# Kernel optimization log

Measured on AMD Instinct MI355X. Metric: run time of the kernel, lower is better.

## Reference

```python
import jax, jax.numpy as jnp
import numpy as np

B = 8192          # batch size
D = 1024          # embedding dim
N_CLASSES = 7     # 7 emotion labels


def setup_inputs() -> dict:
    key = jax.random.key(0)
    k1, k2, k3, k4 = jax.random.split(key, 4)
    return {
        "label": jax.random.randint(k1, (B,), 0, N_CLASSES),
        "s_t": jax.random.normal(k2, (B, D), dtype=jnp.float32),
        "s_v": jax.random.normal(k3, (B, D), dtype=jnp.float32),
        "s_a": jax.random.normal(k4, (B, D), dtype=jnp.float32),
    }


def _single_modal_loss(label, anchor, a_cls, a_m, m_1, m_2):
    # anchor embedding and its norm
    anc = a_m[anchor]                                  # [D]
    anc_norm = jnp.linalg.norm(anc)
    # batched cosine similarity of anchor vs every row of m_1 and m_2
    def cos(m):
        return (m @ anc) / (jnp.linalg.norm(m, axis=1) * anc_norm)  # [B]
    c = cos(m_1) + cos(m_2)                            # [B]
    not_anchor = jnp.arange(label.shape[0]) != anchor
    same = label == label[anchor]
    pos_mask = not_anchor & same
    neg_mask = not_anchor & ~same
    # original code normalizes by full class count (anchor included)
    pos_num = jnp.sum(label == a_cls).astype(c.dtype)
    neg_num = label.shape[0] - pos_num
    pos_score = jnp.sum(jnp.where(pos_mask, c, 0.0)) / pos_num
    neg_score = jnp.sum(jnp.where(neg_mask, c, 0.0)) / neg_num
    return 2.0 - pos_score + neg_score


def reference(label, s_t, s_v, s_a):
    # first class (starting from 0) with more than one sample, like the while loop
    counts = jax.ops.segment_sum(jnp.ones_like(label), label, num_segments=N_CLASSES)
    a_cls = jnp.argmax(counts > 1)
    # deterministic anchor: first index of that class
    anchor = jnp.argmax(label == a_cls)
    t1 = _single_modal_loss(label, anchor, a_cls, s_t, s_v, s_a)
    t2 = _single_modal_loss(label, anchor, a_cls, s_a, s_t, s_v)
    t3 = _single_modal_loss(label, anchor, a_cls, s_v, s_a, s_t)
    return (t1 + t2 + t3) / 3.0
```

## Files before the change

kernel.cpp:

```cpp
#include <hip/hip_runtime.h>

#define NCLS 7

struct Hdr {
    int   anchor;
    int   a_cls;
    float pos_num;
    float neg_num;
    float inv_at;
    float inv_av;
    float inv_aa;
    int   pad;
};

__device__ __forceinline__ float dot4(float4 a, float4 b) {
    return a.x * b.x + a.y * b.y + a.z * b.z + a.w * b.w;
}

__device__ __forceinline__ float wave_fsum_dpp(float x) {
    float t;
    t = __int_as_float(__builtin_amdgcn_update_dpp(0, __float_as_int(x), 0x111, 0xf, 0xf, true));  x += t;
    t = __int_as_float(__builtin_amdgcn_update_dpp(0, __float_as_int(x), 0x112, 0xf, 0xf, true));  x += t;
    t = __int_as_float(__builtin_amdgcn_update_dpp(0, __float_as_int(x), 0x114, 0xf, 0xf, true));  x += t;
    t = __int_as_float(__builtin_amdgcn_update_dpp(0, __float_as_int(x), 0x118, 0xf, 0xf, true));  x += t;
    t = __int_as_float(__builtin_amdgcn_update_dpp(0, __float_as_int(x), 0x142, 0xa, 0xf, false)); x += t;
    t = __int_as_float(__builtin_amdgcn_update_dpp(0, __float_as_int(x), 0x143, 0xc, 0xf, false)); x += t;
    return __int_as_float(__builtin_amdgcn_readlane(__float_as_int(x), 63));
}

__device__ __forceinline__ int wave_isum_dpp(int x) {
    int t;
    t = __builtin_amdgcn_update_dpp(0, x, 0x111, 0xf, 0xf, true);  x += t;
    t = __builtin_amdgcn_update_dpp(0, x, 0x112, 0xf, 0xf, true);  x += t;
    t = __builtin_amdgcn_update_dpp(0, x, 0x114, 0xf, 0xf, true);  x += t;
    t = __builtin_amdgcn_update_dpp(0, x, 0x118, 0xf, 0xf, true);  x += t;
    t = __builtin_amdgcn_update_dpp(0, x, 0x142, 0xa, 0xf, false); x += t;
    t = __builtin_amdgcn_update_dpp(0, x, 0x143, 0xc, 0xf, false); x += t;
    return __builtin_amdgcn_readlane(x, 63);
}

__device__ __forceinline__ int wave_imin_dpp(int x) {
    const int I = 0x7fffffff;
    int t;
    t = __builtin_amdgcn_update_dpp(I, x, 0x111, 0xf, 0xf, false); x = min(x, t);
    t = __builtin_amdgcn_update_dpp(I, x, 0x112, 0xf, 0xf, false); x = min(x, t);
    t = __builtin_amdgcn_update_dpp(I, x, 0x114, 0xf, 0xf, false); x = min(x, t);
    t = __builtin_amdgcn_update_dpp(I, x, 0x118, 0xf, 0xf, false); x = min(x, t);
    t = __builtin_amdgcn_update_dpp(I, x, 0x142, 0xa, 0xf, false); x = min(x, t);
    t = __builtin_amdgcn_update_dpp(I, x, 0x143, 0xc, 0xf, false); x = min(x, t);
    return __builtin_amdgcn_readlane(x, 63);
}

__global__ __launch_bounds__(1024) void prep_kernel(
    const int* __restrict__ label,
    const float* __restrict__ s_t,
    const float* __restrict__ s_v,
    const float* __restrict__ s_a,
    int B, int D, float* __restrict__ ws)
{
    const int tid  = threadIdx.x;
    const int w    = tid >> 6;
    const int lane = tid & 63;

    int cnt[NCLS];
    int mn[NCLS];
#pragma unroll
    for (int k = 0; k < NCLS; ++k) { cnt[k] = 0; mn[k] = 0x7fffffff; }

    const int4* lab4 = (const int4*)label;
    const int n4 = B >> 2;
    for (int j = tid; j < n4; j += 1024) {
        int4 L = lab4[j];
        const int base = j << 2;
        int ls[4] = { L.x, L.y, L.z, L.w };
#pragma unroll
        for (int e = 0; e < 4; ++e) {
#pragma unroll
            for (int k = 0; k < NCLS; ++k) {
                if (ls[e] == k) { cnt[k]++; mn[k] = min(mn[k], base + e); }
            }
        }
    }
    for (int i = (n4 << 2) + tid; i < B; i += 1024) {
        int l = label[i];
#pragma unroll
        for (int k = 0; k < NCLS; ++k)
            if (l == k) { cnt[k]++; mn[k] = min(mn[k], i); }
    }

#pragma unroll
    for (int k = 0; k < NCLS; ++k) {
        cnt[k] = wave_isum_dpp(cnt[k]);
        mn[k]  = wave_imin_dpp(mn[k]);
    }

    __shared__ int   s_cnt[16][NCLS], s_mn[16][NCLS];
    __shared__ int   s_anchor;
    __shared__ float s_norm[12];
    if (lane == 0) {
#pragma unroll
        for (int k = 0; k < NCLS; ++k) { s_cnt[w][k] = cnt[k]; s_mn[w][k] = mn[k]; }
    }
    __syncthreads();

    if (tid == 0) {
        int hist[NCLS], mini[NCLS];
#pragma unroll
        for (int k = 0; k < NCLS; ++k) {
            int hc = 0, mc = 0x7fffffff;
            for (int q = 0; q < 16; ++q) { hc += s_cnt[q][k]; mc = min(mc, s_mn[q][k]); }
            hist[k] = hc; mini[k] = mc;
        }
        int c = 0;
#pragma unroll
        for (int k = NCLS - 1; k >= 0; --k) if (hist[k] > 1) c = k;
        s_anchor = mini[c];

        Hdr* h = (Hdr*)ws;
        h->anchor  = mini[c];
        h->a_cls   = c;
        float pn   = (float)hist[c];
        h->pos_num = pn;
        h->neg_num = (float)B - pn;
    }
    __syncthreads();

    const int anchor = s_anchor;
    if (w < 12) {
        const int rw = w >> 2, qw = w & 3;
        const float* src = (rw == 0) ? s_t : (rw == 1) ? s_v : s_a;
        const float4* row = (const float4*)(src + (size_t)anchor * D);
        const int nvec = D >> 2;
        float s = 0.f;
        for (int j = qw * 64 + lane; j < nvec; j += 256) {
            float4 x = row[j];
            s += dot4(x, x);
        }
        s = wave_fsum_dpp(s);
        if (lane == 0) s_norm[w] = s;
    }
    __syncthreads();
    if (tid < 3)
        ((float*)ws)[4 + tid] = rsqrtf(s_norm[4 * tid] + s_norm[4 * tid + 1] +
                                       s_norm[4 * tid + 2] + s_norm[4 * tid + 3]);
}

__global__ __launch_bounds__(256, 8) void main_kernel(
    const int* __restrict__ label,
    const float* __restrict__ s_t,
    const float* __restrict__ s_v,
    const float* __restrict__ s_a,
    int B, int D, float* __restrict__ ws)
{
    const Hdr* h = (const Hdr*)ws;
    float2* partials = (float2*)(ws + 16);

    const int lane = threadIdx.x & 63;
    const int r    = blockIdx.x * 4 + (threadIdx.x >> 6);
    if (r >= B) return;

    const int anchor = h->anchor;
    const int lab    = label[r];

    const float4* rt = (const float4*)(s_t + (size_t)r * D);
    const float4* rv = (const float4*)(s_v + (size_t)r * D);
    const float4* ra = (const float4*)(s_a + (size_t)r * D);
    const float4* at = (const float4*)(s_t + (size_t)anchor * D);
    const float4* av = (const float4*)(s_v + (size_t)anchor * D);
    const float4* aa = (const float4*)(s_a + (size_t)anchor * D);

    float dt_a = 0.f, dt_v = 0.f, sq_t = 0.f;
    float dv_t = 0.f, dv_a = 0.f, sq_v = 0.f;
    float da_t = 0.f, da_v = 0.f, sq_a = 0.f;

    const int nvec = D >> 2;
#pragma unroll 1
    for (int j = lane; j < nvec; j += 64) {
        float4 t  = rt[j], v  = rv[j], a  = ra[j];
        float4 bt = at[j], bv = av[j], ba = aa[j];
        dt_a += dot4(t, ba);  dt_v += dot4(t, bv);  sq_t += dot4(t, t);
        dv_t += dot4(v, bt);  dv_a += dot4(v, ba);  sq_v += dot4(v, v);
        da_t += dot4(a, bt);  da_v += dot4(a, bv);  sq_a += dot4(a, a);
    }

    const float inv_t = rsqrtf(wave_fsum_dpp(sq_t));
    const float inv_v = rsqrtf(wave_fsum_dpp(sq_v));
    const float inv_a = rsqrtf(wave_fsum_dpp(sq_a));

    float c = inv_t * (dt_a * h->inv_aa + dt_v * h->inv_av)
            + inv_v * (dv_t * h->inv_at + dv_a * h->inv_aa)
            + inv_a * (da_t * h->inv_at + da_v * h->inv_av);
    const float rowtot = wave_fsum_dpp(c);

    if (lane == 0) {
        bool isPos = (lab == h->a_cls) && (r != anchor);
        bool isNeg = (lab != h->a_cls);
        partials[r] = make_float2(isPos ? rowtot : 0.f, isNeg ? rowtot : 0.f);
    }
}

__global__ __launch_bounds__(1024) void finish_kernel(
    const float* __restrict__ ws, int B, float* __restrict__ out)
{
    const Hdr* h = (const Hdr*)ws;
    const float4* p4 = (const float4*)(ws + 16);

    float p = 0.f, n = 0.f;
    const int n4 = B >> 1;
    for (int j = threadIdx.x; j < n4; j += 1024) {
        float4 x = p4[j];
        p += x.x + x.z;
        n += x.y + x.w;
    }
    p = wave_fsum_dpp(p);
    n = wave_fsum_dpp(n);

    __shared__ float pp[16], nn[16];
    const int w = threadIdx.x >> 6, lane = threadIdx.x & 63;
    if (lane == 0) { pp[w] = p; nn[w] = n; }
    __syncthreads();
    if (threadIdx.x == 0) {
        float P = 0.f, N = 0.f;
#pragma unroll
        for (int k = 0; k < 16; ++k) { P += pp[k]; N += nn[k]; }
        out[0] = (6.0f - P / h->pos_num + N / h->neg_num) / 3.0f;
    }
}

extern "C" void kernel_launch(void* const* d_in, const int* in_sizes, int n_in,
                              void* d_out, int out_size, void* d_ws, size_t ws_size,
                              hipStream_t stream) {
    const int*   label = (const int*)d_in[0];
    const float* s_t   = (const float*)d_in[1];
    const float* s_v   = (const float*)d_in[2];
    const float* s_a   = (const float*)d_in[3];

    const int B = in_sizes[0];
    const int D = in_sizes[1] / B;

    float* ws  = (float*)d_ws;
    float* out = (float*)d_out;

    const int nblocks = (B + 3) / 4;

    prep_kernel<<<1, 1024, 0, stream>>>(label, s_t, s_v, s_a, B, D, ws);
    main_kernel<<<nblocks, 256, 0, stream>>>(label, s_t, s_v, s_a, B, D, ws);
    finish_kernel<<<1, 1024, 0, stream>>>(ws, B, out);
}
```

Measured before the change: 29.72 us.

## Fuse label histogram and anchor-norm prep into main kernel, drop prep launch

Removes the single-block prep kernel. Each main block now recomputes the class histogram and first-index scan over all labels itself, and every wave recomputes the anchor row norms alongside its dot products. The row loads are issued up front into registers, before the label scan, so memory latency overlaps that work, and occupancy is lowered to 4 blocks per SIMD to make room for the registers. The cost is redundant label scanning (32KB per block, 2048 blocks) and extra anchor-norm FLOPs in every wave.

```diff
diff --git a/kernel.cpp b/kernel.cpp
--- a/kernel.cpp
+++ b/kernel.cpp
@@ -51,37 +51,55 @@
     return __builtin_amdgcn_readlane(x, 63);
 }
 
-__global__ __launch_bounds__(1024) void prep_kernel(
+__global__ __launch_bounds__(256, 4) void main_kernel(
     const int* __restrict__ label,
     const float* __restrict__ s_t,
     const float* __restrict__ s_v,
     const float* __restrict__ s_a,
     int B, int D, float* __restrict__ ws)
 {
+    float2* partials = (float2*)(ws + 16);
+
     const int tid  = threadIdx.x;
     const int w    = tid >> 6;
     const int lane = tid & 63;
-
-    int cnt[NCLS];
-    int mn[NCLS];
+    const int r    = blockIdx.x * 4 + w;
+
+    const int nvec = D >> 2;
+    const bool fast = (nvec == 256) && (r < B);
+
+    const float4* rt = (const float4*)(s_t + (size_t)r * D);
+    const float4* rv = (const float4*)(s_v + (size_t)r * D);
+    const float4* ra = (const float4*)(s_a + (size_t)r * D);
+
+    float4 T[4], V[4], A[4];
+    if (fast) {
+#pragma unroll
+        for (int it = 0; it < 4; ++it) {
+            const int j = lane + (it << 6);
+            T[it] = rt[j];  V[it] = rv[j];  A[it] = ra[j];
+        }
+    }
+    const int lab = (r < B) ? label[r] : 0;
+
+    int cnt[NCLS], mn[NCLS];
 #pragma unroll
     for (int k = 0; k < NCLS; ++k) { cnt[k] = 0; mn[k] = 0x7fffffff; }
 
     const int4* lab4 = (const int4*)label;
     const int n4 = B >> 2;
-    for (int j = tid; j < n4; j += 1024) {
+    for (int j = tid; j < n4; j += 256) {
         int4 L = lab4[j];
         const int base = j << 2;
         int ls[4] = { L.x, L.y, L.z, L.w };
 #pragma unroll
         for (int e = 0; e < 4; ++e) {
 #pragma unroll
-            for (int k = 0; k < NCLS; ++k) {
+            for (int k = 0; k < NCLS; ++k)
                 if (ls[e] == k) { cnt[k]++; mn[k] = min(mn[k], base + e); }
-            }
-        }
-    }
-    for (int i = (n4 << 2) + tid; i < B; i += 1024) {
+        }
+    }
+    for (int i = (n4 << 2) + tid; i < B; i += 256) {
         int l = label[i];
 #pragma unroll
         for (int k = 0; k < NCLS; ++k)
@@ -94,77 +112,29 @@
         mn[k]  = wave_imin_dpp(mn[k]);
     }
 
-    __shared__ int   s_cnt[16][NCLS], s_mn[16][NCLS];
-    __shared__ int   s_anchor;
-    __shared__ float s_norm[12];
+    __shared__ int s_cnt[4][NCLS], s_mn[4][NCLS];
     if (lane == 0) {
 #pragma unroll
         for (int k = 0; k < NCLS; ++k) { s_cnt[w][k] = cnt[k]; s_mn[w][k] = mn[k]; }
     }
     __syncthreads();
 
-    if (tid == 0) {
-        int hist[NCLS], mini[NCLS];
-#pragma unroll
-        for (int k = 0; k < NCLS; ++k) {
-            int hc = 0, mc = 0x7fffffff;
-            for (int q = 0; q < 16; ++q) { hc += s_cnt[q][k]; mc = min(mc, s_mn[q][k]); }
-            hist[k] = hc; mini[k] = mc;
-        }
-        int c = 0;
-#pragma unroll
-        for (int k = NCLS - 1; k >= 0; --k) if (hist[k] > 1) c = k;
-        s_anchor = mini[c];
-
-        Hdr* h = (Hdr*)ws;
-        h->anchor  = mini[c];
-        h->a_cls   = c;
-        float pn   = (float)hist[c];
-        h->pos_num = pn;
-        h->neg_num = (float)B - pn;
-    }
-    __syncthreads();
-
-    const int anchor = s_anchor;
-    if (w < 12) {
-        const int rw = w >> 2, qw = w & 3;
-        const float* src = (rw == 0) ? s_t : (rw == 1) ? s_v : s_a;
-        const float4* row = (const float4*)(src + (size_t)anchor * D);
-        const int nvec = D >> 2;
-        float s = 0.f;
-        for (int j = qw * 64 + lane; j < nvec; j += 256) {
-            float4 x = row[j];
-            s += dot4(x, x);
-        }
-        s = wave_fsum_dpp(s);
-        if (lane == 0) s_norm[w] = s;
-    }
-    __syncthreads();
-    if (tid < 3)
-        ((float*)ws)[4 + tid] = rsqrtf(s_norm[4 * tid] + s_norm[4 * tid + 1] +
-                                       s_norm[4 * tid + 2] + s_norm[4 * tid + 3]);
-}
-
-__global__ __launch_bounds__(256, 8) void main_kernel(
-    const int* __restrict__ label,
-    const float* __restrict__ s_t,
-    const float* __restrict__ s_v,
-    const float* __restrict__ s_a,
-    int B, int D, float* __restrict__ ws)
-{
-    const Hdr* h = (const Hdr*)ws;
-    float2* partials = (float2*)(ws + 16);
-
-    const int lane = threadIdx.x & 63;
-    const int r    = blockIdx.x * 4 + (threadIdx.x >> 6);
+    int c = 0;
+#pragma unroll
+    for (int k = NCLS - 1; k >= 0; --k) {
+        int hc = s_cnt[0][k] + s_cnt[1][k] + s_cnt[2][k] + s_cnt[3][k];
+        if (hc > 1) c = k;
+    }
+    const int acls   = c;
+    const int posn   = s_cnt[0][c] + s_cnt[1][c] + s_cnt[2][c] + s_cnt[3][c];
+    const int anchor = min(min(s_mn[0][c], s_mn[1][c]), min(s_mn[2][c], s_mn[3][c]));
+
+    if (blockIdx.x == 0 && tid == 0) {
+        ws[2] = (float)posn;
+        ws[3] = (float)(B - posn);
+    }
     if (r >= B) return;
 
-    const int anchor = h->anchor;
-    const int lab    = label[r];
-
-    const float4* rt = (const float4*)(s_t + (size_t)r * D);
-    const float4* rv = (const float4*)(s_v + (size_t)r * D);
-    const float4* ra = (const float4*)(s_a + (size_t)r * D);
     const float4* at = (const float4*)(s_t + (size_t)anchor * D);
     const float4* av = (const float4*)(s_v + (size_t)anchor * D);
     const float4* aa = (const float4*)(s_a + (size_t)anchor * D);
@@ -172,29 +142,45 @@
     float dt_a = 0.f, dt_v = 0.f, sq_t = 0.f;
     float dv_t = 0.f, dv_a = 0.f, sq_v = 0.f;
     float da_t = 0.f, da_v = 0.f, sq_a = 0.f;
-
-    const int nvec = D >> 2;
+    float qa_t = 0.f, qa_v = 0.f, qa_a = 0.f;
+
+    if (fast) {
+#pragma unroll
+        for (int it = 0; it < 4; ++it) {
+            const int j = lane + (it << 6);
+            float4 bt = at[j], bv = av[j], ba = aa[j];
+            dt_a += dot4(T[it], ba);  dt_v += dot4(T[it], bv);  sq_t += dot4(T[it], T[it]);
+            dv_t += dot4(V[it], bt);  dv_a += dot4(V[it], ba);  sq_v += dot4(V[it], V[it]);
+            da_t += dot4(A[it], bt);  da_v += dot4(A[it], bv);  sq_a += dot4(A[it], A[it]);
+            qa_t += dot4(bt, bt);     qa_v += dot4(bv, bv);     qa_a += dot4(ba, ba);
+        }
+    } else {
 #pragma unroll 1
-    for (int j = lane; j < nvec; j += 64) {
-        float4 t  = rt[j], v  = rv[j], a  = ra[j];
-        float4 bt = at[j], bv = av[j], ba = aa[j];
-        dt_a += dot4(t, ba);  dt_v += dot4(t, bv);  sq_t += dot4(t, t);
-        dv_t += dot4(v, bt);  dv_a += dot4(v, ba);  sq_v += dot4(v, v);
-        da_t += dot4(a, bt);  da_v += dot4(a, bv);  sq_a += dot4(a, a);
-    }
-
-    const float inv_t = rsqrtf(wave_fsum_dpp(sq_t));
-    const float inv_v = rsqrtf(wave_fsum_dpp(sq_v));
-    const float inv_a = rsqrtf(wave_fsum_dpp(sq_a));
-
-    float c = inv_t * (dt_a * h->inv_aa + dt_v * h->inv_av)
-            + inv_v * (dv_t * h->inv_at + dv_a * h->inv_aa)
-            + inv_a * (da_t * h->inv_at + da_v * h->inv_av);
-    const float rowtot = wave_fsum_dpp(c);
+        for (int j = lane; j < nvec; j += 64) {
+            float4 t  = rt[j], v  = rv[j], a  = ra[j];
+            float4 bt = at[j], bv = av[j], ba = aa[j];
+            dt_a += dot4(t, ba);  dt_v += dot4(t, bv);  sq_t += dot4(t, t);
+            dv_t += dot4(v, bt);  dv_a += dot4(v, ba);  sq_v += dot4(v, v);
+            da_t += dot4(a, bt);  da_v += dot4(a, bv);  sq_a += dot4(a, a);
+            qa_t += dot4(bt, bt); qa_v += dot4(bv, bv); qa_a += dot4(ba, ba);
+        }
+    }
+
+    const float inv_t  = rsqrtf(wave_fsum_dpp(sq_t));
+    const float inv_v  = rsqrtf(wave_fsum_dpp(sq_v));
+    const float inv_a  = rsqrtf(wave_fsum_dpp(sq_a));
+    const float inv_at = rsqrtf(wave_fsum_dpp(qa_t));
+    const float inv_av = rsqrtf(wave_fsum_dpp(qa_v));
+    const float inv_aa = rsqrtf(wave_fsum_dpp(qa_a));
+
+    float cc = inv_t * (dt_a * inv_aa + dt_v * inv_av)
+             + inv_v * (dv_t * inv_at + dv_a * inv_aa)
+             + inv_a * (da_t * inv_at + da_v * inv_av);
+    const float rowtot = wave_fsum_dpp(cc);
 
     if (lane == 0) {
-        bool isPos = (lab == h->a_cls) && (r != anchor);
-        bool isNeg = (lab != h->a_cls);
+        bool isPos = (lab == acls) && (r != anchor);
+        bool isNeg = (lab != acls);
         partials[r] = make_float2(isPos ? rowtot : 0.f, isNeg ? rowtot : 0.f);
     }
 }
@@ -243,7 +229,6 @@
 
     const int nblocks = (B + 3) / 4;
 
-    prep_kernel<<<1, 1024, 0, stream>>>(label, s_t, s_v, s_a, B, D, ws);
     main_kernel<<<nblocks, 256, 0, stream>>>(label, s_t, s_v, s_a, B, D, ws);
     finish_kernel<<<1, 1024, 0, stream>>>(ws, B, out);
 }
```

New measurement: 39.11 us. 31.6% more time.
